# Kernel tuning notes

Hardware: AMD Instinct MI355X
Metric: run time of the kernel (lower is better)

## Reference

```python
import jax, jax.numpy as jnp
import numpy as np

B, S, D, H = 4, 2048, 1024, 16
HD = D // H  # head dim = 64


def setup_inputs() -> dict:
    key = jax.random.key(0)
    k1, k2, k3 = jax.random.split(key, 3)
    scale = 1.0 / np.sqrt(D).astype(np.float32)
    x = jax.random.normal(k1, (B, S, D), dtype=jnp.float32)
    # q/k slices of nn.MultiheadAttention's in_proj (v and out_proj never
    # influence the returned values since x_t is discarded by forward)
    wq = jax.random.normal(k2, (D, D), dtype=jnp.float32) * scale
    wk = jax.random.normal(k3, (D, D), dtype=jnp.float32) * scale
    bq = jnp.zeros((D,), dtype=jnp.float32)
    bk = jnp.zeros((D,), dtype=jnp.float32)
    # 8 contiguous scale blocks of 256 tokens; last boundary == S
    scales_idx = (jnp.arange(1, 9, dtype=jnp.int64) * (S // 8))
    return {"x": x, "wq": wq, "wk": wk, "bq": bq, "bk": bk,
            "scales_idx": scales_idx}


def reference(x, wq, wk, bq, bk, scales_idx):
    b, s, d = x.shape
    # project q, k and split heads: [B, H, S, HD]
    q = (x @ wq.T + bq).reshape(b, s, H, HD).transpose(0, 2, 1, 3)
    k = (x @ wk.T + bk).reshape(b, s, H, HD).transpose(0, 2, 1, 3)
    inv_sqrt_hd = jnp.asarray(1.0 / np.sqrt(HD), dtype=x.dtype)
    scores = jnp.einsum('bhqd,bhkd->bhqk', q, k) * inv_sqrt_hd  # [B,H,S,S]
    # block-diagonal mask: token i belongs to the block whose right boundary
    # is the first scales_idx entry strictly greater than i
    pos = jnp.arange(s)
    seg = jnp.searchsorted(scales_idx, pos, side='right')  # [S]
    allowed = seg[:, None] == seg[None, :]                  # [S,S] bool
    scores = jnp.where(allowed[None, None], scores, -jnp.inf)
    w = jax.nn.softmax(scores, axis=-1)  # every row has >=1 allowed entry
    weights_attn = jnp.mean(w, axis=1)   # average over heads -> [B,S,S]
    return (x, weights_attn)
```

## Files before the change

### kernel.cpp

```cpp
#include <hip/hip_runtime.h>
#include <hip/hip_bf16.h>
#include <math.h>

#define BB 4
#define SS 2048
#define DD 1024
#define HH 16
#define HD 64
#define MM (BB*SS)
#define NN (2*DD)

typedef __attribute__((ext_vector_type(8))) short short8;
typedef __attribute__((ext_vector_type(4))) float f32x4;
typedef unsigned short ushort_t;

__device__ __forceinline__ void gload16(const void* g, void* l) {
    __builtin_amdgcn_global_load_lds((const __attribute__((address_space(1))) unsigned int*)g,
                                     (__attribute__((address_space(3))) unsigned int*)l,
                                     16, 0, 0);
}

__global__ __launch_bounds__(256)
void copy_cast(const float* __restrict__ x, float* __restrict__ out_x,
               __hip_bfloat16* __restrict__ xb, int n8)
{
    int i = blockIdx.x * 256 + threadIdx.x;
    if (i >= n8) return;
    const float4* s = (const float4*)x + (size_t)i * 2;
    float4 a = s[0], b = s[1];
    float4* o = (float4*)out_x + (size_t)i * 2;
    o[0] = a; o[1] = b;
    __hip_bfloat16 tmp[8];
    tmp[0] = __float2bfloat16(a.x); tmp[1] = __float2bfloat16(a.y);
    tmp[2] = __float2bfloat16(a.z); tmp[3] = __float2bfloat16(a.w);
    tmp[4] = __float2bfloat16(b.x); tmp[5] = __float2bfloat16(b.y);
    tmp[6] = __float2bfloat16(b.z); tmp[7] = __float2bfloat16(b.w);
    *(float4*)&xb[(size_t)i * 8] = *(float4*)tmp;
}

__global__ __launch_bounds__(256)
void cast_w(const float* __restrict__ wq, const float* __restrict__ wk,
            __hip_bfloat16* __restrict__ wb)
{
    const int half = (DD * DD) / 8;
    int i = blockIdx.x * 256 + threadIdx.x;
    if (i >= 2 * half) return;
    const float* src = (i < half) ? wq : wk;
    int j = (i < half) ? i : i - half;
    const float4* s = (const float4*)src + (size_t)j * 2;
    float4 a = s[0], b = s[1];
    __hip_bfloat16 tmp[8];
    tmp[0] = __float2bfloat16(a.x); tmp[1] = __float2bfloat16(a.y);
    tmp[2] = __float2bfloat16(a.z); tmp[3] = __float2bfloat16(a.w);
    tmp[4] = __float2bfloat16(b.x); tmp[5] = __float2bfloat16(b.y);
    tmp[6] = __float2bfloat16(b.z); tmp[7] = __float2bfloat16(b.w);
    *(float4*)&wb[(size_t)i * 8] = *(float4*)tmp;
}

__global__ __launch_bounds__(256, 2)
void proj_mfma(const ushort_t* __restrict__ xb, const ushort_t* __restrict__ wb,
               const float* __restrict__ bq, const float* __restrict__ bk,
               __hip_bfloat16* __restrict__ Qh, __hip_bfloat16* __restrict__ Kh)
{
    __shared__ __align__(16) ushort_t As[128 * 64];
    __shared__ __align__(16) ushort_t Bs[128 * 64];

    const int t = threadIdx.x;
    const int wv = t >> 6, lane = t & 63, quad = lane >> 4, l15 = lane & 15;
    const int m0 = blockIdx.x * 128, n0 = blockIdx.y * 128;
    const int wm = (wv & 1) * 64, wn = (wv >> 1) * 64;

    f32x4 acc[4][4];
    #pragma unroll
    for (int mt = 0; mt < 4; ++mt)
        #pragma unroll
        for (int nt = 0; nt < 4; ++nt) acc[mt][nt] = (f32x4){0.f, 0.f, 0.f, 0.f};

    for (int kt = 0; kt < DD; kt += 64) {
        __syncthreads();
        #pragma unroll
        for (int call = 0; call < 4; ++call) {
            int c = call * 256 + t;
            int row = c >> 3, ch = c & 7;
            int gch = ch ^ (row & 7);
            gload16(xb + (size_t)(m0 + row) * DD + kt + gch * 8,
                    As + ((size_t)call * 256 + wv * 64) * 8);
            gload16(wb + (size_t)(n0 + row) * DD + kt + gch * 8,
                    Bs + ((size_t)call * 256 + wv * 64) * 8);
        }
        __syncthreads();
        #pragma unroll
        for (int ks = 0; ks < 2; ++ks) {
            short8 a[4], bb_[4];
            #pragma unroll
            for (int mt = 0; mt < 4; ++mt) {
                int r = wm + mt * 16 + l15;
                int sl = r * 8 + ((ks * 4 + quad) ^ (r & 7));
                a[mt] = *(const short8*)&As[sl * 8];
            }
            #pragma unroll
            for (int nt = 0; nt < 4; ++nt) {
                int r = wn + nt * 16 + l15;
                int sl = r * 8 + ((ks * 4 + quad) ^ (r & 7));
                bb_[nt] = *(const short8*)&Bs[sl * 8];
            }
            #pragma unroll
            for (int mt = 0; mt < 4; ++mt)
                #pragma unroll
                for (int nt = 0; nt < 4; ++nt)
                    acc[mt][nt] = __builtin_amdgcn_mfma_f32_16x16x32_bf16(
                        a[mt], bb_[nt], acc[mt][nt], 0, 0, 0);
        }
    }

    const bool isQ = (n0 < DD);
    const float* bias = isQ ? bq : bk;
    __hip_bfloat16* outp = isQ ? Qh : Kh;
    const int nc0 = isQ ? n0 : (n0 - DD);
    #pragma unroll
    for (int nt = 0; nt < 4; ++nt) {
        const int nc = nc0 + wn + nt * 16 + l15;
        const int h = nc >> 6, hd = nc & 63;
        const float bv = bias[nc];
        #pragma unroll
        for (int mt = 0; mt < 4; ++mt)
            #pragma unroll
            for (int reg = 0; reg < 4; ++reg) {
                int m = m0 + wm + mt * 16 + quad * 4 + reg;
                int b = m >> 11, s = m & 2047;
                outp[(((size_t)(b * HH + h)) * SS + s) * HD + hd] =
                    __float2bfloat16(acc[mt][nt][reg] + bv);
            }
    }
}

__global__ __launch_bounds__(256, 2)
void attn_reg(const ushort_t* __restrict__ Qh, const ushort_t* __restrict__ Kh,
              const int* __restrict__ scales, float* __restrict__ outw)
{
    __shared__ float comb[16][256];

    const int gid = blockIdx.x;
    const int xcd = gid & 7, slot = gid >> 3;
    const int rt = slot & 15;
    const int group = ((slot >> 4) << 3) | xcd;
    const int bb = group >> 3, blk = group & 7;
    const int start = blk ? scales[blk - 1] : 0;

    const int t = threadIdx.x;
    const int wv = t >> 6, lane = t & 63, quad = lane >> 4, l15 = lane & 15;

    const int qrow0 = start + rt * 16;
    const int ko = quad * 8;

    f32x4 accm[16];
    #pragma unroll
    for (int nt = 0; nt < 16; ++nt) accm[nt] = (f32x4){0.f, 0.f, 0.f, 0.f};

    for (int hh = 0; hh < 4; ++hh) {
        const int h = wv * 4 + hh;
        const size_t headbase = ((size_t)(bb * HH + h)) * SS;
        const ushort_t* Qrow = Qh + (headbase + qrow0 + l15) * HD + ko;
        const ushort_t* Kblk = Kh + (headbase + start + l15) * HD + ko;

        short8 af0 = *(const short8*)(Qrow);
        short8 af1 = *(const short8*)(Qrow + 32);

        f32x4 sc[16];
        #pragma unroll
        for (int nt = 0; nt < 16; ++nt) {
            const ushort_t* kp = Kblk + (size_t)(nt * 16) * HD;
            short8 b0 = *(const short8*)(kp);
            short8 b1 = *(const short8*)(kp + 32);
            f32x4 s = (f32x4){0.f, 0.f, 0.f, 0.f};
            s = __builtin_amdgcn_mfma_f32_16x16x32_bf16(af0, b0, s, 0, 0, 0);
            s = __builtin_amdgcn_mfma_f32_16x16x32_bf16(af1, b1, s, 0, 0, 0);
            sc[nt] = s;
        }

        float rs[4] = {0.f, 0.f, 0.f, 0.f};
        #pragma unroll
        for (int nt = 0; nt < 16; ++nt) {
            #pragma unroll
            for (int r = 0; r < 4; ++r) {
                float p = __expf(sc[nt][r] * 0.125f);
                sc[nt][r] = p;
                rs[r] += p;
            }
        }
        #pragma unroll
        for (int r = 0; r < 4; ++r) {
            #pragma unroll
            for (int off = 1; off < 16; off <<= 1) rs[r] += __shfl_xor(rs[r], off, 64);
            rs[r] = 1.0f / rs[r];
        }
        #pragma unroll
        for (int nt = 0; nt < 16; ++nt)
            #pragma unroll
            for (int r = 0; r < 4; ++r) accm[nt][r] += sc[nt][r] * rs[r];
    }

    if (wv == 0) {
        #pragma unroll
        for (int nt = 0; nt < 16; ++nt)
            #pragma unroll
            for (int r = 0; r < 4; ++r)
                comb[quad * 4 + r][nt * 16 + l15] = accm[nt][r];
    }
    __syncthreads();
    #pragma unroll
    for (int w = 1; w < 4; ++w) {
        if (wv == w) {
            #pragma unroll
            for (int nt = 0; nt < 16; ++nt)
                #pragma unroll
                for (int r = 0; r < 4; ++r)
                    comb[quad * 4 + r][nt * 16 + l15] += accm[nt][r];
        }
        __syncthreads();
    }

    const float s16 = 1.0f / (float)HH;
    const size_t orow0 = (size_t)bb * SS + qrow0;
    #pragma unroll
    for (int it = 0; it < 32; ++it) {
        int flat = it * 256 + t;
        int row = flat >> 9;
        int col = (flat & 511) * 4;
        float4 v = make_float4(0.f, 0.f, 0.f, 0.f);
        unsigned lc = (unsigned)(col - start);
        if (lc < 256u) {
            const float* c = &comb[row][lc];
            v = make_float4(c[0] * s16, c[1] * s16, c[2] * s16, c[3] * s16);
        }
        *(float4*)&outw[(orow0 + row) * SS + col] = v;
    }
}

extern "C" void kernel_launch(void* const* d_in, const int* in_sizes, int n_in,
                              void* d_out, int out_size, void* d_ws, size_t ws_size,
                              hipStream_t stream)
{
    const float* x  = (const float*)d_in[0];
    const float* wq = (const float*)d_in[1];
    const float* wk = (const float*)d_in[2];
    const float* bq = (const float*)d_in[3];
    const float* bk = (const float*)d_in[4];
    const int* scales = (const int*)d_in[5];

    float* out_x = (float*)d_out;
    float* out_w = out_x + (size_t)BB * SS * DD;

    char* w = (char*)d_ws;
    __hip_bfloat16* xb = (__hip_bfloat16*)(w);
    __hip_bfloat16* wb = (__hip_bfloat16*)(w + 16777216);
    __hip_bfloat16* Qh = (__hip_bfloat16*)(w + 20971520);
    __hip_bfloat16* Kh = (__hip_bfloat16*)(w + 37748736);

    copy_cast<<<4096, 256, 0, stream>>>(x, out_x, xb, (MM * DD) / 8);
    cast_w<<<1024, 256, 0, stream>>>(wq, wk, wb);

    dim3 pgrid(MM / 128, NN / 128);
    proj_mfma<<<pgrid, 256, 0, stream>>>((const ushort_t*)xb, (const ushort_t*)wb,
                                         bq, bk, Qh, Kh);

    attn_reg<<<512, 256, 0, stream>>>((const ushort_t*)Qh, (const ushort_t*)Kh,
                                      scales, out_w);
}
```

Measured before the change: 218.6 us.

## Split heads across blocks with atomic accumulation and move output zero-fill into prep

```diff
diff --git a/kernel.cpp b/kernel.cpp
--- a/kernel.cpp
+++ b/kernel.cpp
@@ -20,41 +20,50 @@
                                      16, 0, 0);
 }
 
+#define PREP_Z  16384
+#define PREP_X  4096
+#define PREP_W  1024
+
 __global__ __launch_bounds__(256)
-void copy_cast(const float* __restrict__ x, float* __restrict__ out_x,
-               __hip_bfloat16* __restrict__ xb, int n8)
-{
-    int i = blockIdx.x * 256 + threadIdx.x;
-    if (i >= n8) return;
-    const float4* s = (const float4*)x + (size_t)i * 2;
-    float4 a = s[0], b = s[1];
-    float4* o = (float4*)out_x + (size_t)i * 2;
-    o[0] = a; o[1] = b;
-    __hip_bfloat16 tmp[8];
-    tmp[0] = __float2bfloat16(a.x); tmp[1] = __float2bfloat16(a.y);
-    tmp[2] = __float2bfloat16(a.z); tmp[3] = __float2bfloat16(a.w);
-    tmp[4] = __float2bfloat16(b.x); tmp[5] = __float2bfloat16(b.y);
-    tmp[6] = __float2bfloat16(b.z); tmp[7] = __float2bfloat16(b.w);
-    *(float4*)&xb[(size_t)i * 8] = *(float4*)tmp;
-}
-
-__global__ __launch_bounds__(256)
-void cast_w(const float* __restrict__ wq, const float* __restrict__ wk,
-            __hip_bfloat16* __restrict__ wb)
-{
-    const int half = (DD * DD) / 8;
-    int i = blockIdx.x * 256 + threadIdx.x;
-    if (i >= 2 * half) return;
-    const float* src = (i < half) ? wq : wk;
-    int j = (i < half) ? i : i - half;
-    const float4* s = (const float4*)src + (size_t)j * 2;
-    float4 a = s[0], b = s[1];
-    __hip_bfloat16 tmp[8];
-    tmp[0] = __float2bfloat16(a.x); tmp[1] = __float2bfloat16(a.y);
-    tmp[2] = __float2bfloat16(a.z); tmp[3] = __float2bfloat16(a.w);
-    tmp[4] = __float2bfloat16(b.x); tmp[5] = __float2bfloat16(b.y);
-    tmp[6] = __float2bfloat16(b.z); tmp[7] = __float2bfloat16(b.w);
-    *(float4*)&wb[(size_t)i * 8] = *(float4*)tmp;
+void prep(const float* __restrict__ x, const float* __restrict__ wq,
+          const float* __restrict__ wk, float* __restrict__ out_x,
+          float* __restrict__ out_w, __hip_bfloat16* __restrict__ xb,
+          __hip_bfloat16* __restrict__ wb)
+{
+    const int bid = blockIdx.x, t = threadIdx.x;
+    if (bid < PREP_Z) {
+        size_t idx = (size_t)bid * 256 + t;
+        *(float4*)&out_w[idx * 4] = make_float4(0.f, 0.f, 0.f, 0.f);
+        return;
+    }
+    if (bid < PREP_Z + PREP_X) {
+        size_t i = (size_t)(bid - PREP_Z) * 256 + t;
+        const float4* s = (const float4*)x + i * 2;
+        float4 a = s[0], b = s[1];
+        float4* o = (float4*)out_x + i * 2;
+        o[0] = a; o[1] = b;
+        __hip_bfloat16 tmp[8];
+        tmp[0] = __float2bfloat16(a.x); tmp[1] = __float2bfloat16(a.y);
+        tmp[2] = __float2bfloat16(a.z); tmp[3] = __float2bfloat16(a.w);
+        tmp[4] = __float2bfloat16(b.x); tmp[5] = __float2bfloat16(b.y);
+        tmp[6] = __float2bfloat16(b.z); tmp[7] = __float2bfloat16(b.w);
+        *(float4*)&xb[i * 8] = *(float4*)tmp;
+        return;
+    }
+    {
+        const int half = (DD * DD) / 8;
+        size_t i = (size_t)(bid - PREP_Z - PREP_X) * 256 + t;
+        const float* src = (i < (size_t)half) ? wq : wk;
+        size_t j = (i < (size_t)half) ? i : i - half;
+        const float4* s = (const float4*)src + j * 2;
+        float4 a = s[0], b = s[1];
+        __hip_bfloat16 tmp[8];
+        tmp[0] = __float2bfloat16(a.x); tmp[1] = __float2bfloat16(a.y);
+        tmp[2] = __float2bfloat16(a.z); tmp[3] = __float2bfloat16(a.w);
+        tmp[4] = __float2bfloat16(b.x); tmp[5] = __float2bfloat16(b.y);
+        tmp[6] = __float2bfloat16(b.z); tmp[7] = __float2bfloat16(b.w);
+        *(float4*)&wb[i * 8] = *(float4*)tmp;
+    }
 }
 
 __global__ __launch_bounds__(256, 2)
@@ -134,31 +143,33 @@
     }
 }
 
-__global__ __launch_bounds__(256, 2)
-void attn_reg(const ushort_t* __restrict__ Qh, const ushort_t* __restrict__ Kh,
-              const int* __restrict__ scales, float* __restrict__ outw)
-{
-    __shared__ float comb[16][256];
+#define CSTR 260
+
+__global__ __launch_bounds__(256, 4)
+void attn_atomic(const ushort_t* __restrict__ Qh, const ushort_t* __restrict__ Kh,
+                 const int* __restrict__ scales, float* __restrict__ outw)
+{
+    __shared__ float comb[16 * CSTR];
 
     const int gid = blockIdx.x;
     const int xcd = gid & 7, slot = gid >> 3;
     const int rt = slot & 15;
-    const int group = ((slot >> 4) << 3) | xcd;
+    const int hs = (slot >> 4) & 1;
+    const int group = ((slot >> 5) << 3) | xcd;
     const int bb = group >> 3, blk = group & 7;
     const int start = blk ? scales[blk - 1] : 0;
 
     const int t = threadIdx.x;
     const int wv = t >> 6, lane = t & 63, quad = lane >> 4, l15 = lane & 15;
-
     const int qrow0 = start + rt * 16;
     const int ko = quad * 8;
 
-    f32x4 accm[16];
-    #pragma unroll
-    for (int nt = 0; nt < 16; ++nt) accm[nt] = (f32x4){0.f, 0.f, 0.f, 0.f};
-
-    for (int hh = 0; hh < 4; ++hh) {
-        const int h = wv * 4 + hh;
+    for (int i = t; i < 16 * CSTR; i += 256) comb[i] = 0.f;
+    __syncthreads();
+
+    #pragma unroll
+    for (int hh = 0; hh < 2; ++hh) {
+        const int h = hs * 8 + wv * 2 + hh;
         const size_t headbase = ((size_t)(bb * HH + h)) * SS;
         const ushort_t* Qrow = Qh + (headbase + qrow0 + l15) * HD + ko;
         const ushort_t* Kblk = Kh + (headbase + start + l15) * HD + ko;
@@ -192,48 +203,24 @@
         for (int r = 0; r < 4; ++r) {
             #pragma unroll
             for (int off = 1; off < 16; off <<= 1) rs[r] += __shfl_xor(rs[r], off, 64);
-            rs[r] = 1.0f / rs[r];
-        }
-        #pragma unroll
-        for (int nt = 0; nt < 16; ++nt)
-            #pragma unroll
-            for (int r = 0; r < 4; ++r) accm[nt][r] += sc[nt][r] * rs[r];
-    }
-
-    if (wv == 0) {
-        #pragma unroll
-        for (int nt = 0; nt < 16; ++nt)
+            rs[r] = (1.0f / 16.0f) / rs[r];
+        }
+        #pragma unroll
+        for (int nt = 0; nt < 16; ++nt) {
             #pragma unroll
             for (int r = 0; r < 4; ++r)
-                comb[quad * 4 + r][nt * 16 + l15] = accm[nt][r];
+                atomicAdd(&comb[(quad * 4 + r) * CSTR + nt * 16 + l15],
+                          sc[nt][r] * rs[r]);
+        }
     }
     __syncthreads();
-    #pragma unroll
-    for (int w = 1; w < 4; ++w) {
-        if (wv == w) {
-            #pragma unroll
-            for (int nt = 0; nt < 16; ++nt)
-                #pragma unroll
-                for (int r = 0; r < 4; ++r)
-                    comb[quad * 4 + r][nt * 16 + l15] += accm[nt][r];
-        }
-        __syncthreads();
-    }
-
-    const float s16 = 1.0f / (float)HH;
-    const size_t orow0 = (size_t)bb * SS + qrow0;
-    #pragma unroll
-    for (int it = 0; it < 32; ++it) {
-        int flat = it * 256 + t;
-        int row = flat >> 9;
-        int col = (flat & 511) * 4;
-        float4 v = make_float4(0.f, 0.f, 0.f, 0.f);
-        unsigned lc = (unsigned)(col - start);
-        if (lc < 256u) {
-            const float* c = &comb[row][lc];
-            v = make_float4(c[0] * s16, c[1] * s16, c[2] * s16, c[3] * s16);
-        }
-        *(float4*)&outw[(orow0 + row) * SS + col] = v;
+
+    const size_t obase = ((size_t)bb * SS + qrow0) * SS + start;
+    #pragma unroll
+    for (int it = 0; it < 16; ++it) {
+        int idx = it * 256 + t;
+        int r = idx >> 8, c = idx & 255;
+        unsafeAtomicAdd(&outw[obase + (size_t)r * SS + c], comb[r * CSTR + c]);
     }
 }
 
@@ -257,13 +244,12 @@
     __hip_bfloat16* Qh = (__hip_bfloat16*)(w + 20971520);
     __hip_bfloat16* Kh = (__hip_bfloat16*)(w + 37748736);
 
-    copy_cast<<<4096, 256, 0, stream>>>(x, out_x, xb, (MM * DD) / 8);
-    cast_w<<<1024, 256, 0, stream>>>(wq, wk, wb);
+    prep<<<PREP_Z + PREP_X + PREP_W, 256, 0, stream>>>(x, wq, wk, out_x, out_w, xb, wb);
 
     dim3 pgrid(MM / 128, NN / 128);
     proj_mfma<<<pgrid, 256, 0, stream>>>((const ushort_t*)xb, (const ushort_t*)wb,
                                          bq, bk, Qh, Kh);
 
-    attn_reg<<<512, 256, 0, stream>>>((const ushort_t*)Qh, (const ushort_t*)Kh,
-                                      scales, out_w);
-}
+    attn_atomic<<<1024, 256, 0, stream>>>((const ushort_t*)Qh, (const ushort_t*)Kh,
+                                          scales, out_w);
+}
```

After: 357.6 us. 1.64x slower.
